# Performance work log

Hardware: AMD Instinct MI355X
Metric: run time of the kernel (lower is better)

## Reference

```python
import jax, jax.numpy as jnp
import numpy as np


def setup_inputs() -> dict:
    key = jax.random.key(0)
    ks = jax.random.split(key, 12)
    B, Nq, Ns, NODES = 128, 16, 256, 3
    V, E, C, H, OUT, NA = 50000, 300, 1024, 8, 300, 5000
    s = 0.05
    return {
        "he_ques": jax.random.randint(ks[0], (B, Nq, NODES), 0, V),
        "he_kg": jax.random.randint(ks[1], (B, Ns, NODES), 0, V),
        "emb": jax.random.normal(ks[2], (V, E), jnp.float32) * s,
        "q2h_w": jax.random.normal(ks[3], (C, E * NODES), jnp.float32) * s,
        "q2h_b": jax.random.normal(ks[4], (C,), jnp.float32) * s,
        "k2h_w": jax.random.normal(ks[5], (C, E * NODES), jnp.float32) * s,
        "k2h_b": jax.random.normal(ks[6], (C,), jnp.float32) * s,
        "h2att_w": jax.random.normal(ks[7], (H, C), jnp.float32) * s,
        "h2att_b": jax.random.normal(ks[8], (H,), jnp.float32) * s,
        "fc_w": jax.random.normal(ks[9], (OUT, C * H), jnp.float32) * s,
        "fc_b": jax.random.normal(ks[10], (OUT,), jnp.float32) * s,
        "glove_cands": jax.random.normal(ks[11], (NA, OUT), jnp.float32) * s,
    }


def reference(he_ques, he_kg, emb, q2h_w, q2h_b, k2h_w, k2h_b,
              h2att_w, h2att_b, fc_w, fc_b, glove_cands):
    B, Nq, _ = he_ques.shape
    Ns = he_kg.shape[1]
    H, C = h2att_w.shape
    # embed node indices and flatten per-hyperedge: [B, N, nodes*E]
    hq = emb[he_ques].reshape(B, Nq, -1)
    hs = emb[he_kg].reshape(B, Ns, -1)
    # linear projections (dropout p=0 in eval)
    hq = hq @ q2h_w.T + q2h_b  # [B, Nq, C]
    hs = hs @ k2h_w.T + k2h_b  # [B, Ns, C]
    # bilinear attention logits: h2att(outer(hq, hs)) fused into one einsum
    # logits[b,h,q,s] = sum_c hq[b,q,c] * hs[b,s,c] * W[h,c] + b[h]
    logits = jnp.einsum('bqc,bsc,hc->bhqs', hq, hs, h2att_w) + h2att_b[None, :, None, None]
    att = jax.nn.softmax(logits.reshape(B, H, Nq * Ns), axis=2).reshape(B, H, Nq, Ns)
    # per-head bilinear readout (replaces the per-head repeat+matmul loop):
    # out[b,h,c] = sum_{q,s} hq[b,q,c] * att[b,h,q,s] * hs[b,s,c]
    pooled = jnp.einsum('bqc,bhqs,bsc->bhc', hq, att, hs).reshape(B, H * C)
    out = pooled @ fc_w.T + fc_b  # [B, n_out]
    sim = out @ glove_cands.T  # [B, n_ans]
    return jax.nn.log_softmax(sim, axis=1)
```

## Files before the change

### kernel.cpp

```cpp
#include <hip/hip_runtime.h>
#include <stdint.h>


typedef short s16x8 __attribute__((ext_vector_type(8)));
typedef float f32x4 __attribute__((ext_vector_type(4)));

#define ASYNC_CP16(gsrc, ldst)                                                  \
  __builtin_amdgcn_global_load_lds(                                             \
      (const __attribute__((address_space(1))) void*)(gsrc),                    \
      (__attribute__((address_space(3))) void*)(ldst), 16, 0, 0)

__device__ __forceinline__ float bfr2f(uint16_t u) {
  return __builtin_bit_cast(float, (uint32_t)u << 16);
}
__device__ __forceinline__ uint16_t f2bfr(float f) {
  uint32_t u = __builtin_bit_cast(uint32_t, f);
  u += 0x7fffu + ((u >> 16) & 1u);
  return (uint16_t)(u >> 16);
}

__global__ __launch_bounds__(256) void cvt_all(
    const float* __restrict__ emb_f, const float* __restrict__ wk_f,
    const float* __restrict__ wq_f, const float* __restrict__ glove_f,
    const float* __restrict__ watt_f,
    uint16_t* __restrict__ EMB, uint16_t* __restrict__ WK,
    uint16_t* __restrict__ WQ, uint16_t* __restrict__ GLV,
    uint16_t* __restrict__ WATT) {
  const int idx = blockIdx.x * 256 + threadIdx.x;
  const int TOT = 61264 * 80;
  if (idx < TOT) {
    const int row = idx / 80, j = idx % 80;
    const float* src;
    uint16_t* dst;
    int srow, svalid;
    if (row < 50000) {
      src = emb_f; dst = EMB; srow = row; svalid = 1;
    } else if (row < 53072) {
      src = wk_f; dst = WK + (size_t)(row - 50000) * 0; srow = row - 50000;
      dst = WK; svalid = 1;
    } else if (row < 56144) {
      src = wq_f; dst = WQ; srow = row - 53072; svalid = 1;
    } else {
      src = glove_f; dst = GLV; srow = row - 56144; svalid = (srow < 5000);
    }
    float4 v = make_float4(0.f, 0.f, 0.f, 0.f);
    if (svalid && j < 75) v = *(const float4*)(src + (size_t)srow * 300 + j * 4);
    ushort4 o;
    o.x = f2bfr(v.x); o.y = f2bfr(v.y); o.z = f2bfr(v.z); o.w = f2bfr(v.w);
    const int drow = (row < 50000) ? row : srow;
    *(ushort4*)(dst + (size_t)drow * 320 + j * 4) = o;
  } else {
    const int i = idx - TOT;
    if (i < 1024) {
      float4 a = *(const float4*)(watt_f + i * 8);
      float4 b = *(const float4*)(watt_f + i * 8 + 4);
      ushort4 o0, o1;
      o0.x = f2bfr(a.x); o0.y = f2bfr(a.y); o0.z = f2bfr(a.z); o0.w = f2bfr(a.w);
      o1.x = f2bfr(b.x); o1.y = f2bfr(b.y); o1.z = f2bfr(b.z); o1.w = f2bfr(b.w);
      *(ushort4*)(WATT + i * 8) = o0;
      *(ushort4*)(WATT + i * 8 + 4) = o1;
    }
  }
}

__global__ __launch_bounds__(256) void cvt_fc(const float* __restrict__ src,
                                              uint16_t* __restrict__ dst) {
  int i4 = blockIdx.x * 256 + threadIdx.x;
  int pos = i4 * 4;
  int r = pos >> 13, c = pos & 8191;
  float4 v = make_float4(0.f, 0.f, 0.f, 0.f);
  if (r < 300) v = *(const float4*)(src + (size_t)r * 8192 + c);
  ushort4 o;
  o.x = f2bfr(v.x); o.y = f2bfr(v.y); o.z = f2bfr(v.z); o.w = f2bfr(v.w);
  *(ushort4*)(dst + (size_t)r * 8192 + c) = o;
}

__global__ __launch_bounds__(256) void gemm_gather2(
    const int* __restrict__ heK, const int* __restrict__ heQ,
    const uint16_t* __restrict__ emb,
    const uint16_t* __restrict__ WKp, const uint16_t* __restrict__ WQp,
    const float* __restrict__ bK, const float* __restrict__ bQ,
    uint16_t* __restrict__ HS, uint16_t* __restrict__ HQ) {
  __shared__ uint16_t ring[3 * 8192];
  __shared__ int sIdx[384];
  char* ringB = (char*)ring;

  const int t = threadIdx.x;
  const int lane = t & 63, wave = t >> 6;
  const int wr = wave >> 1, wc = wave & 1;
  const int fr = lane & 15, fq = lane >> 4;
  const int srow = t >> 2, skg = t & 3;
  const int skg2 = skg ^ ((srow >> 1) & 3);

  const int v = blockIdx.x + 8 * blockIdx.y;
  const int w = (v & 7) * 272 + (v >> 3);
  const int bx = w & 7, by = w >> 3;
  const int n0 = bx * 128;
  const bool isK = by < 256;
  const int m0 = (isK ? by : by - 256) * 128;
  const int* he = isK ? heK : heQ;
  const uint16_t* W = isK ? WKp : WQp;
  const float* bias = isK ? bK : bQ;
  uint16_t* C = isK ? HS : HQ;

  for (int i = t; i < 384; i += 256) sIdx[i] = he[(long)m0 * 3 + i];
  __syncthreads();

  uint32_t ea[2][3];
#pragma unroll
  for (int h = 0; h < 2; h++)
#pragma unroll
    for (int nd = 0; nd < 3; nd++)
      ea[h][nd] =
          (uint32_t)sIdx[(h * 64 + srow) * 3 + nd] * 640u + (uint32_t)(skg2 * 16);
  const uint16_t* Wr0 = W + (long)(n0 + srow) * 960 + skg2 * 8;
  const uint16_t* Wr1 = W + (long)(n0 + 64 + srow) * 960 + skg2 * 8;

  f32x4 zv = {0.f, 0.f, 0.f, 0.f};
  f32x4 acc[4][4];
#pragma unroll
  for (int i = 0; i < 4; i++)
#pragma unroll
    for (int j = 0; j < 4; j++) acc[i][j] = zv;

  int snd = 0, skk = 0, sk = 0, sbuf = 0;
  auto STAGE = [&]() {
    const int bb = sbuf * 16384;
    const uint32_t e0 = snd == 0 ? ea[0][0] : (snd == 1 ? ea[0][1] : ea[0][2]);
    const uint32_t e1 = snd == 0 ? ea[1][0] : (snd == 1 ? ea[1][1] : ea[1][2]);
    ASYNC_CP16((const char*)emb + e0 + skk * 64, ringB + bb + t * 16);
    ASYNC_CP16((const char*)emb + e1 + skk * 64, ringB + bb + 4096 + t * 16);
    ASYNC_CP16(Wr0 + sk, ringB + bb + 8192 + t * 16);
    ASYNC_CP16(Wr1 + sk, ringB + bb + 12288 + t * 16);
    sk += 32;
    if (++skk == 10) { skk = 0; ++snd; }
    if (++sbuf == 3) sbuf = 0;
  };

  STAGE();
  STAGE();

  const int fsw = (fq ^ ((fr >> 1) & 3)) * 8;
  int aof[4], bof[4];
#pragma unroll
  for (int mi = 0; mi < 4; mi++) aof[mi] = (wr * 64 + mi * 16 + fr) * 32 + fsw;
#pragma unroll
  for (int ni = 0; ni < 4; ni++)
    bof[ni] = 4096 + (wc * 64 + ni * 16 + fr) * 32 + fsw;

  int cbuf = 0;
  for (int kt = 0; kt < 30; ++kt) {
    if (kt < 28) STAGE();
    if (kt < 28)      asm volatile("s_waitcnt vmcnt(8)" ::: "memory");
    else if (kt < 29) asm volatile("s_waitcnt vmcnt(4)" ::: "memory");
    else              asm volatile("s_waitcnt vmcnt(0)" ::: "memory");
    __builtin_amdgcn_s_barrier();
    asm volatile("" ::: "memory");
    const uint16_t* base = ring + cbuf * 8192;
    s16x8 af[4], bv[4];
#pragma unroll
    for (int mi = 0; mi < 4; mi++) af[mi] = *(const s16x8*)(base + aof[mi]);
#pragma unroll
    for (int ni = 0; ni < 4; ni++) bv[ni] = *(const s16x8*)(base + bof[ni]);
    __builtin_amdgcn_s_setprio(1);
#pragma unroll
    for (int mi = 0; mi < 4; mi++)
#pragma unroll
      for (int ni = 0; ni < 4; ni++)
        acc[mi][ni] = __builtin_amdgcn_mfma_f32_16x16x32_bf16(
            af[mi], bv[ni], acc[mi][ni], 0, 0, 0);
    __builtin_amdgcn_s_setprio(0);
    asm volatile("s_waitcnt lgkmcnt(0)" ::: "memory");
    __builtin_amdgcn_s_barrier();
    if (++cbuf == 3) cbuf = 0;
  }

#pragma unroll
  for (int ni = 0; ni < 4; ni++) {
    const int gn = n0 + wc * 64 + ni * 16 + fr;
    const float bval = bias[gn];
#pragma unroll
    for (int mi = 0; mi < 4; mi++) {
      const int gmb = m0 + wr * 64 + mi * 16 + fq * 4;
      uint16_t* cp = C + (long)gmb * 1024 + gn;
      cp[0]    = f2bfr(acc[mi][ni][0] + bval);
      cp[1024] = f2bfr(acc[mi][ni][1] + bval);
      cp[2048] = f2bfr(acc[mi][ni][2] + bval);
      cp[3072] = f2bfr(acc[mi][ni][3] + bval);
    }
  }
}

__global__ __launch_bounds__(256) void gemm_logits(
    const uint16_t* __restrict__ hq, const uint16_t* __restrict__ watt,
    const uint16_t* __restrict__ hs, uint16_t* __restrict__ att) {
  __shared__ uint16_t ring[3 * 4096];
  char* ringB = (char*)ring;

  const int t = threadIdx.x;
  const int lane = t & 63, wave = t >> 6;
  const int wr = wave >> 1, wc = wave & 1;
  const int fr = lane & 15, fq = lane >> 4;
  const int srow = t >> 2, skg = t & 3;
  const int skg2 = skg ^ ((srow >> 1) & 3);

  int bx = blockIdx.x, bz = blockIdx.z;
  {
    const int v = bx + 2 * bz;
    const int w = (v & 7) * 32 + (v >> 3);
    bx = w & 1;
    bz = w >> 1;
  }
  const int n0 = bx * 128;

  const uint16_t* Bs0 = hs + (long)bz * 262144 + (long)(n0 + srow) * 1024 + skg2 * 8;
  const uint16_t* Bs1 = hs + (long)bz * 262144 + (long)(n0 + 64 + srow) * 1024 + skg2 * 8;
  const uint16_t* hqp = hq + (long)(bz * 16 + fr) * 1024 + fq * 8;
  const uint16_t* wp0 = watt + (long)(wr * 4 + 0) * 1024 + fq * 8;
  const uint16_t* wp1 = watt + (long)(wr * 4 + 1) * 1024 + fq * 8;
  const uint16_t* wp2 = watt + (long)(wr * 4 + 2) * 1024 + fq * 8;
  const uint16_t* wp3 = watt + (long)(wr * 4 + 3) * 1024 + fq * 8;

  f32x4 zv = {0.f, 0.f, 0.f, 0.f};
  f32x4 acc[4][4];
#pragma unroll
  for (int i = 0; i < 4; i++)
#pragma unroll
    for (int j = 0; j < 4; j++) acc[i][j] = zv;

  int sbuf = 0, cbuf = 0;
  ASYNC_CP16(Bs0, ringB + t * 16);
  ASYNC_CP16(Bs1, ringB + 2048 + t * 16);
  ASYNC_CP16(Bs0 + 32, ringB + 4096 + t * 16);
  ASYNC_CP16(Bs1 + 32, ringB + 4096 + 2048 + t * 16);
  sbuf = 2;
  s16x8 hqA = *(const s16x8*)(hqp);
  s16x8 wA0 = *(const s16x8*)(wp0), wA1 = *(const s16x8*)(wp1);
  s16x8 wA2 = *(const s16x8*)(wp2), wA3 = *(const s16x8*)(wp3);
  s16x8 hqB, wB0, wB1, wB2, wB3;

  const int fsw = (fq ^ ((fr >> 1) & 3)) * 8;
  int bof[4];
#pragma unroll
  for (int ni = 0; ni < 4; ni++)
    bof[ni] = (wc * 64 + ni * 16 + fr) * 32 + fsw;

#define LOG_BODY(KT, HQS, W0S, W1S, W2S, W3S, HQD, W0D, W1D, W2D, W3D)          \
  {                                                                             \
    const int kt = (KT);                                                        \
    if (kt + 2 < 32) {                                                          \
      ASYNC_CP16(Bs0 + (kt + 2) * 32, ringB + sbuf * 4096 + t * 16);            \
      ASYNC_CP16(Bs1 + (kt + 2) * 32, ringB + sbuf * 4096 + 2048 + t * 16);     \
      if (++sbuf == 3) sbuf = 0;                                                \
    }                                                                           \
    if (kt + 1 < 32) {                                                          \
      const int ko = (kt + 1) * 32;                                             \
      HQD = *(const s16x8*)(hqp + ko);                                          \
      W0D = *(const s16x8*)(wp0 + ko); W1D = *(const s16x8*)(wp1 + ko);         \
      W2D = *(const s16x8*)(wp2 + ko); W3D = *(const s16x8*)(wp3 + ko);         \
    }                                                                           \
    asm volatile("s_waitcnt vmcnt(7)" ::: "memory");                            \
    __builtin_amdgcn_s_barrier();                                               \
    asm volatile("" ::: "memory");                                              \
    s16x8 af0, af1, af2, af3, bv[4];                                            \
    _Pragma("unroll") for (int j = 0; j < 8; j++) {                             \
      const float hv = bfr2f((uint16_t)HQS[j]);                                 \
      af0[j] = (short)f2bfr(hv * bfr2f((uint16_t)W0S[j]));                      \
      af1[j] = (short)f2bfr(hv * bfr2f((uint16_t)W1S[j]));                      \
      af2[j] = (short)f2bfr(hv * bfr2f((uint16_t)W2S[j]));                      \
      af3[j] = (short)f2bfr(hv * bfr2f((uint16_t)W3S[j]));                      \
    }                                                                           \
    const uint16_t* base = ring + cbuf * 4096;                                  \
    _Pragma("unroll") for (int ni = 0; ni < 4; ni++)                            \
        bv[ni] = *(const s16x8*)(base + bof[ni]);                               \
    __builtin_amdgcn_s_setprio(1);                                              \
    _Pragma("unroll") for (int ni = 0; ni < 4; ni++) {                          \
      acc[0][ni] = __builtin_amdgcn_mfma_f32_16x16x32_bf16(af0, bv[ni],         \
                                                           acc[0][ni], 0, 0, 0);\
      acc[1][ni] = __builtin_amdgcn_mfma_f32_16x16x32_bf16(af1, bv[ni],         \
                                                           acc[1][ni], 0, 0, 0);\
      acc[2][ni] = __builtin_amdgcn_mfma_f32_16x16x32_bf16(af2, bv[ni],         \
                                                           acc[2][ni], 0, 0, 0);\
      acc[3][ni] = __builtin_amdgcn_mfma_f32_16x16x32_bf16(af3, bv[ni],         \
                                                           acc[3][ni], 0, 0, 0);\
    }                                                                           \
    __builtin_amdgcn_s_setprio(0);                                              \
    asm volatile("s_waitcnt lgkmcnt(0)" ::: "memory");                          \
    __builtin_amdgcn_s_barrier();                                               \
    if (++cbuf == 3) cbuf = 0;                                                  \
  }

  for (int kt2 = 0; kt2 < 32; kt2 += 2) {
    LOG_BODY(kt2, hqA, wA0, wA1, wA2, wA3, hqB, wB0, wB1, wB2, wB3);
    LOG_BODY(kt2 + 1, hqB, wB0, wB1, wB2, wB3, hqA, wA0, wA1, wA2, wA3);
  }
#undef LOG_BODY

#pragma unroll
  for (int ni = 0; ni < 4; ni++) {
    const int gn = n0 + wc * 64 + ni * 16 + fr;
#pragma unroll
    for (int mi = 0; mi < 4; mi++)
#pragma unroll
      for (int j = 0; j < 4; j++) {
        const int gm = wr * 64 + mi * 16 + fq * 4 + j;
        att[(long)bz * 32768 + gm * 256 + gn] = f2bfr(acc[mi][ni][j]);
      }
  }
}

template <int SWZ>
__global__ __launch_bounds__(256) void gemm_pipe(
    const uint16_t* __restrict__ A, int lda, long sAb,
    const uint16_t* __restrict__ Bt, int ldb, long sBb,
    int ksteps, int kchunk,
    float* __restrict__ Cf, int ldcf, int nmax, long sCf) {
  __shared__ uint16_t ring[3 * 8192];
  char* ringB = (char*)ring;

  const int t = threadIdx.x;
  const int lane = t & 63, wave = t >> 6;
  const int wr = wave >> 1, wc = wave & 1;
  const int fr = lane & 15, fq = lane >> 4;
  const int srow = t >> 2, skg = t & 3;
  const int skg2 = skg ^ ((srow >> 1) & 3);

  int bx = blockIdx.x, bz = blockIdx.z;
  if (SWZ) {
    const int nwg = gridDim.x * gridDim.z;
    const int v = bx + gridDim.x * bz;
    const int w = (v & 7) * (nwg >> 3) + (v >> 3);
    bx = w % gridDim.x;
    bz = w / gridDim.x;
  }
  const int m0 = blockIdx.y * 128, n0 = bx * 128;
  const uint16_t* Ab = A + (long)bz * sAb;
  const uint16_t* Bb = Bt;

  f32x4 zv = {0.f, 0.f, 0.f, 0.f};
  f32x4 acc[4][4];
#pragma unroll
  for (int i = 0; i < 4; i++)
#pragma unroll
    for (int j = 0; j < 4; j++) acc[i][j] = zv;

  const long kbase = (long)bz * kchunk;
  const uint16_t* As0 = Ab + (long)(m0 + srow) * lda + kbase + skg2 * 8;
  const uint16_t* As1 = Ab + (long)(m0 + 64 + srow) * lda + kbase + skg2 * 8;
  const uint16_t* Bs0 = Bb + (long)(n0 + srow) * ldb + kbase + skg2 * 8;
  const uint16_t* Bs1 = Bb + (long)(n0 + 64 + srow) * ldb + kbase + skg2 * 8;

  int sk = 0, sbuf = 0;
  auto STAGE = [&]() {
    const int bb = sbuf * 16384;
    ASYNC_CP16(As0 + sk, ringB + bb + t * 16);
    ASYNC_CP16(As1 + sk, ringB + bb + 4096 + t * 16);
    ASYNC_CP16(Bs0 + sk, ringB + bb + 8192 + t * 16);
    ASYNC_CP16(Bs1 + sk, ringB + bb + 12288 + t * 16);
    sk += 32;
    if (++sbuf == 3) sbuf = 0;
  };

  STAGE();
  STAGE();

  const int fsw = (fq ^ ((fr >> 1) & 3)) * 8;
  int aof[4], bof[4];
#pragma unroll
  for (int mi = 0; mi < 4; mi++) aof[mi] = (wr * 64 + mi * 16 + fr) * 32 + fsw;
#pragma unroll
  for (int ni = 0; ni < 4; ni++)
    bof[ni] = 4096 + (wc * 64 + ni * 16 + fr) * 32 + fsw;

  int cbuf = 0;
  for (int kt = 0; kt < ksteps; ++kt) {
    if (kt + 2 < ksteps) STAGE();
    if (kt + 2 < ksteps)      asm volatile("s_waitcnt vmcnt(8)" ::: "memory");
    else if (kt + 1 < ksteps) asm volatile("s_waitcnt vmcnt(4)" ::: "memory");
    else                      asm volatile("s_waitcnt vmcnt(0)" ::: "memory");
    __builtin_amdgcn_s_barrier();
    asm volatile("" ::: "memory");
    const uint16_t* base = ring + cbuf * 8192;
    s16x8 af[4], bv[4];
#pragma unroll
    for (int mi = 0; mi < 4; mi++) af[mi] = *(const s16x8*)(base + aof[mi]);
#pragma unroll
    for (int ni = 0; ni < 4; ni++) bv[ni] = *(const s16x8*)(base + bof[ni]);
#pragma unroll
    for (int mi = 0; mi < 4; mi++)
#pragma unroll
      for (int ni = 0; ni < 4; ni++)
        acc[mi][ni] = __builtin_amdgcn_mfma_f32_16x16x32_bf16(
            af[mi], bv[ni], acc[mi][ni], 0, 0, 0);
    asm volatile("s_waitcnt lgkmcnt(0)" ::: "memory");
    __builtin_amdgcn_s_barrier();
    if (++cbuf == 3) cbuf = 0;
  }

#pragma unroll
  for (int ni = 0; ni < 4; ni++) {
    const int gn = n0 + wc * 64 + ni * 16 + fr;
    if (gn < nmax) {
#pragma unroll
      for (int mi = 0; mi < 4; mi++)
#pragma unroll
        for (int j = 0; j < 4; j++) {
          const int gm = m0 + wr * 64 + mi * 16 + fq * 4 + j;
          Cf[(long)bz * sCf + (long)gm * ldcf + gn] = acc[mi][ni][j];
        }
    }
  }
}

__global__ __launch_bounds__(256) void gemm_pv(
    const uint16_t* __restrict__ att, const uint16_t* __restrict__ hs,
    const uint16_t* __restrict__ hqp, uint16_t* __restrict__ pooled) {
  __shared__ uint16_t sT[128 * 264];
  __shared__ uint16_t sA[4096];
  __shared__ uint16_t sHq[2048];

  const int t = threadIdx.x;
  const int lane = t & 63, wave = t >> 6;
  const int wr = wave >> 1, wc = wave & 1;
  const int fr = lane & 15, fq = lane >> 4;
  const int srow = t >> 2, skg = t & 3;
  const int skg2 = skg ^ ((srow >> 1) & 3);

  int bx = blockIdx.x, bz = blockIdx.z;
  {
    const int v = bx + 8 * bz;
    const int w = (v & 7) * 128 + (v >> 3);
    bx = w & 7;
    bz = w >> 3;
  }
  const int n0 = bx * 128;

  const uint16_t* hsb = hs + (long)bz * 262144;
  const int sloc = t & 15, c8 = t >> 4;
  s16x8 vv[16];
#pragma unroll
  for (int p = 0; p < 16; p++)
    vv[p] = *(const s16x8*)(hsb + (long)(p * 16 + sloc) * 1024 + n0 + c8 * 8);
  *(s16x8*)(sHq + (t >> 4) * 128 + (t & 15) * 8) =
      *(const s16x8*)(hqp + (long)bz * 16384 + (long)(t >> 4) * 1024 + n0 +
                      (t & 15) * 8);
#pragma unroll
  for (int p = 0; p < 16; p++) {
    const int s = p * 16 + sloc;
#pragma unroll
    for (int j = 0; j < 8; j++)
      sT[(c8 * 8 + j) * 264 + s] = (uint16_t)vv[p][j];
  }
  __syncthreads();

  f32x4 zv = {0.f, 0.f, 0.f, 0.f};
  f32x4 acc[4][4];
#pragma unroll
  for (int i = 0; i < 4; i++)
#pragma unroll
    for (int j = 0; j < 4; j++) acc[i][j] = zv;

  const uint16_t* As0 = att + (long)bz * 32768 + (long)srow * 256 + skg2 * 8;
  const uint16_t* As1 = att + (long)bz * 32768 + (long)(64 + srow) * 256 + skg2 * 8;

  const int fsw = (fq ^ ((fr >> 1) & 3)) * 8;
  int aof[4];
#pragma unroll
  for (int mi = 0; mi < 4; mi++) aof[mi] = (wr * 64 + mi * 16 + fr) * 32 + fsw;

  for (int kt = 0; kt < 8; ++kt) {
    ASYNC_CP16(As0 + kt * 32, (char*)sA + t * 16);
    ASYNC_CP16(As1 + kt * 32, (char*)sA + 4096 + t * 16);
    __syncthreads();
    s16x8 af[4], bv[4];
#pragma unroll
    for (int mi = 0; mi < 4; mi++) af[mi] = *(const s16x8*)(sA + aof[mi]);
#pragma unroll
    for (int ni = 0; ni < 4; ni++)
      bv[ni] = *(const s16x8*)(sT + (wc * 64 + ni * 16 + fr) * 264 + kt * 32 +
                               fq * 8);
    __builtin_amdgcn_s_setprio(1);
#pragma unroll
    for (int mi = 0; mi < 4; mi++)
#pragma unroll
      for (int ni = 0; ni < 4; ni++)
        acc[mi][ni] = __builtin_amdgcn_mfma_f32_16x16x32_bf16(
            af[mi], bv[ni], acc[mi][ni], 0, 0, 0);
    __builtin_amdgcn_s_setprio(0);
    __syncthreads();
  }

#pragma unroll
  for (int mi = 0; mi < 4; mi++) {
    const int hh = wr * 4 + mi;
#pragma unroll
    for (int ni = 0; ni < 4; ni++) {
      const int col = wc * 64 + ni * 16 + fr;
      float p = 0.f;
#pragma unroll
      for (int j = 0; j < 4; j++)
        p += acc[mi][ni][j] * bfr2f(sHq[(fq * 4 + j) * 128 + col]);
      p += __shfl_xor(p, 16);
      p += __shfl_xor(p, 32);
      if (fq == 0)
        pooled[(long)bz * 8192 + hh * 1024 + n0 + col] = f2bfr(p);
    }
  }
}

__global__ __launch_bounds__(256) void softmax_att(uint16_t* __restrict__ att) {
  const int b = blockIdx.x >> 3, h = blockIdx.x & 7;
  uint16_t* base = att + (long)b * 32768 + h * 4096;
  const int t = threadIdx.x;
  __shared__ float red[8];
  s16x8 v0 = *(const s16x8*)(base + t * 16);
  s16x8 v1 = *(const s16x8*)(base + t * 16 + 8);
  float f[16];
#pragma unroll
  for (int j = 0; j < 8; j++) {
    f[j] = bfr2f((uint16_t)v0[j]);
    f[8 + j] = bfr2f((uint16_t)v1[j]);
  }
  float mx = f[0];
#pragma unroll
  for (int j = 1; j < 16; j++) mx = fmaxf(mx, f[j]);
#pragma unroll
  for (int d = 1; d < 64; d <<= 1) mx = fmaxf(mx, __shfl_xor(mx, d));
  if ((t & 63) == 0) red[t >> 6] = mx;
  __syncthreads();
  mx = fmaxf(fmaxf(red[0], red[1]), fmaxf(red[2], red[3]));
  float s = 0.f;
#pragma unroll
  for (int j = 0; j < 16; j++) {
    f[j] = __expf(f[j] - mx);
    s += f[j];
  }
#pragma unroll
  for (int d = 1; d < 64; d <<= 1) s += __shfl_xor(s, d);
  if ((t & 63) == 0) red[4 + (t >> 6)] = s;
  __syncthreads();
  const float ri = 1.f / (red[4] + red[5] + red[6] + red[7]);
  s16x8 o0, o1;
#pragma unroll
  for (int j = 0; j < 8; j++) {
    o0[j] = (short)f2bfr(f[j] * ri);
    o1[j] = (short)f2bfr(f[8 + j] * ri);
  }
  *(s16x8*)(base + t * 16) = o0;
  *(s16x8*)(base + t * 16 + 8) = o1;
}

__global__ __launch_bounds__(256) void cvt_out_k(const float* __restrict__ parts,
                                                 const float* __restrict__ fc_b,
                                                 uint16_t* __restrict__ outb) {
  int idx = blockIdx.x * 256 + threadIdx.x;
  if (idx >= 128 * 320) return;
  int m = idx / 320, n = idx % 320;
  float v = 0.f;
  if (n < 300) {
    v = fc_b[n];
#pragma unroll
    for (int ch = 0; ch < 32; ch++) v += parts[ch * 38400 + m * 300 + n];
  }
  outb[idx] = f2bfr(v);
}

__global__ __launch_bounds__(256) void logsoftmax_k(const float* __restrict__ sim,
                                                    float* __restrict__ out) {
  const int r = blockIdx.x, t = threadIdx.x;
  __shared__ float red[4];
  __shared__ float red2[4];
  const float* x = sim + (long)r * 5000;
  float mx = -1e30f;
  for (int i = t; i < 5000; i += 256) mx = fmaxf(mx, x[i]);
#pragma unroll
  for (int d = 1; d < 64; d <<= 1) mx = fmaxf(mx, __shfl_xor(mx, d));
  if ((t & 63) == 0) red[t >> 6] = mx;
  __syncthreads();
  mx = fmaxf(fmaxf(red[0], red[1]), fmaxf(red[2], red[3]));
  float s = 0.f;
  for (int i = t; i < 5000; i += 256) s += __expf(x[i] - mx);
#pragma unroll
  for (int d = 1; d < 64; d <<= 1) s += __shfl_xor(s, d);
  if ((t & 63) == 0) red2[t >> 6] = s;
  __syncthreads();
  s = red2[0] + red2[1] + red2[2] + red2[3];
  const float lse = mx + logf(s);
  float* o = out + (long)r * 5000;
  for (int i = t; i < 5000; i += 256) o[i] = x[i] - lse;
}

extern "C" void kernel_launch(void* const* d_in, const int* in_sizes, int n_in,
                              void* d_out, int out_size, void* d_ws, size_t ws_size,
                              hipStream_t stream) {
  (void)in_sizes; (void)n_in; (void)out_size; (void)ws_size;
  const int* he_q = (const int*)d_in[0];
  const int* he_k = (const int*)d_in[1];
  const float* emb_f = (const float*)d_in[2];
  const float* q2h_w = (const float*)d_in[3];
  const float* q2h_b = (const float*)d_in[4];
  const float* k2h_w = (const float*)d_in[5];
  const float* k2h_b = (const float*)d_in[6];
  const float* h2att_w = (const float*)d_in[7];
  const float* fc_w = (const float*)d_in[9];
  const float* fc_b = (const float*)d_in[10];
  const float* glove = (const float*)d_in[11];
  float* out = (float*)d_out;

  char* ws = (char*)d_ws;
  uint16_t* EMB   = (uint16_t*)(ws);
  uint16_t* WK    = (uint16_t*)(ws + 32000000);
  uint16_t* WQ    = (uint16_t*)(ws + 33966080);
  uint16_t* WATT  = (uint16_t*)(ws + 35932160);
  uint16_t* WFC   = (uint16_t*)(ws + 35948544);
  uint16_t* GLV   = (uint16_t*)(ws + 42240000);
  uint16_t* HQ    = (uint16_t*)(ws + 45516800);
  uint16_t* HS    = (uint16_t*)(ws + 49711104);
  uint16_t* ATT   = (uint16_t*)(ws + 183928832);
  uint16_t* POOL  = (uint16_t*)(ws + 192317440);
  uint16_t* OUTB  = (uint16_t*)(ws + 195643392);
  float*    SIM   = (float*)(ws + 195725312);
  float*    PARTS = (float*)(ws + 49711104);

  cvt_all<<<19149, 256, 0, stream>>>(emb_f, k2h_w, q2h_w, glove, h2att_w,
                                     EMB, WK, WQ, GLV, WATT);
  cvt_fc<<<3072, 256, 0, stream>>>(fc_w, WFC);

  gemm_gather2<<<dim3(8, 272), 256, 0, stream>>>(
      he_k, he_q, EMB, WK, WQ, k2h_b, q2h_b, HS, HQ);

  gemm_logits<<<dim3(2, 1, 128), 256, 0, stream>>>(HQ, WATT, HS, ATT);
  softmax_att<<<1024, 256, 0, stream>>>(ATT);

  gemm_pv<<<dim3(8, 1, 128), 256, 0, stream>>>(ATT, HS, HQ, POOL);

  gemm_pipe<0><<<dim3(3, 1, 32), 256, 0, stream>>>(
      POOL, 8192, 0, WFC, 8192, 0, 8, 256, PARTS, 300, 300, 38400);

  cvt_out_k<<<160, 256, 0, stream>>>(PARTS, fc_b, OUTB);

  gemm_pipe<0><<<dim3(40, 1, 1), 256, 0, stream>>>(
      OUTB, 320, 0, GLV, 320, 0, 10, 0, SIM, 5000, 5000, 0);

  logsoftmax_k<<<128, 256, 0, stream>>>(SIM, out);
}
```

Baseline: 209.0 us.

## Merge fc weight conversion into cvt_all and shrink gather GEMM ring to double buffer

The fc_w fp32-to-bf16 conversion moves into the cvt_all kernel, removing one kernel launch. Separately, the gather GEMM's LDS ring drops from three stages to two, which halves its shared memory. The aim is more resident blocks per CU, at the cost of a shallower prefetch distance that may expose more load latency.

```diff
diff --git a/kernel.cpp b/kernel.cpp
--- a/kernel.cpp
+++ b/kernel.cpp
@@ -22,13 +22,14 @@
 __global__ __launch_bounds__(256) void cvt_all(
     const float* __restrict__ emb_f, const float* __restrict__ wk_f,
     const float* __restrict__ wq_f, const float* __restrict__ glove_f,
-    const float* __restrict__ watt_f,
+    const float* __restrict__ watt_f, const float* __restrict__ fc_f,
     uint16_t* __restrict__ EMB, uint16_t* __restrict__ WK,
     uint16_t* __restrict__ WQ, uint16_t* __restrict__ GLV,
-    uint16_t* __restrict__ WATT) {
+    uint16_t* __restrict__ WATT, uint16_t* __restrict__ WFC) {
   const int idx = blockIdx.x * 256 + threadIdx.x;
-  const int TOT = 61264 * 80;
-  if (idx < TOT) {
+  const int TOT1 = 61264 * 80;
+  const int TOT2 = TOT1 + 1024;
+  if (idx < TOT1) {
     const int row = idx / 80, j = idx % 80;
     const float* src;
     uint16_t* dst;
@@ -36,8 +37,7 @@
     if (row < 50000) {
       src = emb_f; dst = EMB; srow = row; svalid = 1;
     } else if (row < 53072) {
-      src = wk_f; dst = WK + (size_t)(row - 50000) * 0; srow = row - 50000;
-      dst = WK; svalid = 1;
+      src = wk_f; dst = WK; srow = row - 50000; svalid = 1;
     } else if (row < 56144) {
       src = wq_f; dst = WQ; srow = row - 53072; svalid = 1;
     } else {
@@ -47,32 +47,28 @@
     if (svalid && j < 75) v = *(const float4*)(src + (size_t)srow * 300 + j * 4);
     ushort4 o;
     o.x = f2bfr(v.x); o.y = f2bfr(v.y); o.z = f2bfr(v.z); o.w = f2bfr(v.w);
-    const int drow = (row < 50000) ? row : srow;
-    *(ushort4*)(dst + (size_t)drow * 320 + j * 4) = o;
+    *(ushort4*)(dst + (size_t)srow * 320 + j * 4) = o;
+  } else if (idx < TOT2) {
+    const int i = idx - TOT1;
+    float4 a = *(const float4*)(watt_f + i * 8);
+    float4 b = *(const float4*)(watt_f + i * 8 + 4);
+    ushort4 o0, o1;
+    o0.x = f2bfr(a.x); o0.y = f2bfr(a.y); o0.z = f2bfr(a.z); o0.w = f2bfr(a.w);
+    o1.x = f2bfr(b.x); o1.y = f2bfr(b.y); o1.z = f2bfr(b.z); o1.w = f2bfr(b.w);
+    *(ushort4*)(WATT + i * 8) = o0;
+    *(ushort4*)(WATT + i * 8 + 4) = o1;
   } else {
-    const int i = idx - TOT;
-    if (i < 1024) {
-      float4 a = *(const float4*)(watt_f + i * 8);
-      float4 b = *(const float4*)(watt_f + i * 8 + 4);
-      ushort4 o0, o1;
-      o0.x = f2bfr(a.x); o0.y = f2bfr(a.y); o0.z = f2bfr(a.z); o0.w = f2bfr(a.w);
-      o1.x = f2bfr(b.x); o1.y = f2bfr(b.y); o1.z = f2bfr(b.z); o1.w = f2bfr(b.w);
-      *(ushort4*)(WATT + i * 8) = o0;
-      *(ushort4*)(WATT + i * 8 + 4) = o1;
+    const int i4 = idx - TOT2;
+    if (i4 < 384 * 2048) {
+      const int pos = i4 * 4;
+      const int r = pos >> 13, c = pos & 8191;
+      float4 v = make_float4(0.f, 0.f, 0.f, 0.f);
+      if (r < 300) v = *(const float4*)(fc_f + (size_t)r * 8192 + c);
+      ushort4 o;
+      o.x = f2bfr(v.x); o.y = f2bfr(v.y); o.z = f2bfr(v.z); o.w = f2bfr(v.w);
+      *(ushort4*)(WFC + (size_t)r * 8192 + c) = o;
     }
   }
-}
-
-__global__ __launch_bounds__(256) void cvt_fc(const float* __restrict__ src,
-                                              uint16_t* __restrict__ dst) {
-  int i4 = blockIdx.x * 256 + threadIdx.x;
-  int pos = i4 * 4;
-  int r = pos >> 13, c = pos & 8191;
-  float4 v = make_float4(0.f, 0.f, 0.f, 0.f);
-  if (r < 300) v = *(const float4*)(src + (size_t)r * 8192 + c);
-  ushort4 o;
-  o.x = f2bfr(v.x); o.y = f2bfr(v.y); o.z = f2bfr(v.z); o.w = f2bfr(v.w);
-  *(ushort4*)(dst + (size_t)r * 8192 + c) = o;
 }
 
 __global__ __launch_bounds__(256) void gemm_gather2(
@@ -81,7 +77,7 @@
     const uint16_t* __restrict__ WKp, const uint16_t* __restrict__ WQp,
     const float* __restrict__ bK, const float* __restrict__ bQ,
     uint16_t* __restrict__ HS, uint16_t* __restrict__ HQ) {
-  __shared__ uint16_t ring[3 * 8192];
+  __shared__ uint16_t ring[2 * 8192];
   __shared__ int sIdx[384];
   char* ringB = (char*)ring;
 
@@ -134,10 +130,9 @@
     ASYNC_CP16(Wr1 + sk, ringB + bb + 12288 + t * 16);
     sk += 32;
     if (++skk == 10) { skk = 0; ++snd; }
-    if (++sbuf == 3) sbuf = 0;
+    sbuf ^= 1;
   };
 
-  STAGE();
   STAGE();
 
   const int fsw = (fq ^ ((fr >> 1) & 3)) * 8;
@@ -150,10 +145,12 @@
 
   int cbuf = 0;
   for (int kt = 0; kt < 30; ++kt) {
-    if (kt < 28) STAGE();
-    if (kt < 28)      asm volatile("s_waitcnt vmcnt(8)" ::: "memory");
-    else if (kt < 29) asm volatile("s_waitcnt vmcnt(4)" ::: "memory");
-    else              asm volatile("s_waitcnt vmcnt(0)" ::: "memory");
+    if (kt < 29) {
+      STAGE();
+      asm volatile("s_waitcnt vmcnt(4)" ::: "memory");
+    } else {
+      asm volatile("s_waitcnt vmcnt(0)" ::: "memory");
+    }
     __builtin_amdgcn_s_barrier();
     asm volatile("" ::: "memory");
     const uint16_t* base = ring + cbuf * 8192;
@@ -172,7 +169,7 @@
     __builtin_amdgcn_s_setprio(0);
     asm volatile("s_waitcnt lgkmcnt(0)" ::: "memory");
     __builtin_amdgcn_s_barrier();
-    if (++cbuf == 3) cbuf = 0;
+    cbuf ^= 1;
   }
 
 #pragma unroll
@@ -622,9 +619,8 @@
   float*    SIM   = (float*)(ws + 195725312);
   float*    PARTS = (float*)(ws + 49711104);
 
-  cvt_all<<<19149, 256, 0, stream>>>(emb_f, k2h_w, q2h_w, glove, h2att_w,
-                                     EMB, WK, WQ, GLV, WATT);
-  cvt_fc<<<3072, 256, 0, stream>>>(fc_w, WFC);
+  cvt_all<<<22221, 256, 0, stream>>>(emb_f, k2h_w, q2h_w, glove, h2att_w, fc_w,
+                                     EMB, WK, WQ, GLV, WATT, WFC);
 
   gemm_gather2<<<dim3(8, 272), 256, 0, stream>>>(
       he_k, he_q, EMB, WK, WQ, k2h_b, q2h_b, HS, HQ);
```

New measurement: 193.7 us. 7.3% less time.
